# Performance work log

Measured on AMD Instinct MI355X. Metric: run time of the kernel, lower is better.

## Reference

```python
import jax, jax.numpy as jnp
import numpy as np

N_HEAD = 16
N_KV = 4
HEAD_DIM = 128
EPS = 1e-6


def setup_inputs() -> dict:
    key = jax.random.key(0)
    k1, k2, k3 = jax.random.split(key, 3)
    d_model = N_HEAD * HEAD_DIM
    qkv_out = (N_HEAD + 2 * N_KV) * HEAD_DIM
    B, T = 2, 2048
    x = jax.random.normal(k1, (B, T, d_model), dtype=jnp.float32)
    W_qkv = jax.random.normal(k2, (d_model, qkv_out), dtype=jnp.float32) * (d_model ** -0.5)
    W_proj = jax.random.normal(k3, (d_model, d_model), dtype=jnp.float32) * (d_model ** -0.5)
    q_scale = jnp.ones((HEAD_DIM,), dtype=jnp.float32)
    k_scale = jnp.ones((HEAD_DIM,), dtype=jnp.float32)
    return {"x": x, "W_qkv": W_qkv, "W_proj": W_proj, "q_scale": q_scale, "k_scale": k_scale}


def _rms_norm(t):
    return t * jax.lax.rsqrt(jnp.mean(t * t, axis=-1, keepdims=True) + EPS)


def reference(x, W_qkv, W_proj, q_scale, k_scale):
    B, T, C = x.shape
    qkv = x @ W_qkv  # [B, T, (H+2*KV)*D]
    q, k, v = jnp.split(qkv, [N_HEAD * HEAD_DIM, (N_HEAD + N_KV) * HEAD_DIM], axis=-1)
    q = q.reshape(B, T, N_HEAD, HEAD_DIM).transpose(0, 2, 1, 3)  # [B,H,T,D]
    k = k.reshape(B, T, N_KV, HEAD_DIM).transpose(0, 2, 1, 3)    # [B,KV,T,D]
    v = v.reshape(B, T, N_KV, HEAD_DIM).transpose(0, 2, 1, 3)
    # QK RMS-norm with learned per-dim scales
    q = _rms_norm(q) * q_scale
    k = _rms_norm(k) * k_scale
    # GQA: repeat kv heads to match query heads
    rep = N_HEAD // N_KV
    k = jnp.repeat(k, rep, axis=1)
    v = jnp.repeat(v, rep, axis=1)
    # causal SDPA
    scale = 1.0 / jnp.sqrt(jnp.float32(HEAD_DIM))
    scores = jnp.einsum('bhqd,bhkd->bhqk', q, k) * scale
    causal = jnp.tril(jnp.ones((T, T), dtype=bool))
    scores = jnp.where(causal, scores, jnp.finfo(scores.dtype).min)
    attn = jax.nn.softmax(scores, axis=-1)
    y = jnp.einsum('bhqk,bhkd->bhqd', attn, v)  # [B,H,T,D]
    y = y.transpose(0, 2, 1, 3).reshape(B, T, C)
    return y @ W_proj
```

## Files before the change

kernel.cpp:

```cpp
#include <hip/hip_runtime.h>

typedef __bf16 bf16;
typedef __bf16 bf16x8 __attribute__((ext_vector_type(8)));
typedef __bf16 bf16x4 __attribute__((ext_vector_type(4)));
typedef float f32x4 __attribute__((ext_vector_type(4)));
typedef float f32x16 __attribute__((ext_vector_type(16)));
typedef unsigned u32x4 __attribute__((ext_vector_type(4)));

#define EXP2F(x) __builtin_amdgcn_exp2f(x)

#define LOAD_LDS16(gp, lp)                                                     \
  __builtin_amdgcn_global_load_lds(                                            \
      (const __attribute__((address_space(1))) void*)(gp),                     \
      (__attribute__((address_space(3))) void*)(lp), 16, 0, 0)

__global__ __launch_bounds__(256) void k_pre(const float* __restrict__ x,
                                             const float* __restrict__ Wqkv,
                                             bf16* __restrict__ xb,
                                             bf16* __restrict__ Wqkvt) {
  int bid = blockIdx.x, tid = threadIdx.x;
  if (bid < 4096) {
    int i = bid * 256 + tid;
    float4 v0 = ((const float4*)x)[2 * i];
    float4 v1 = ((const float4*)x)[2 * i + 1];
    bf16x8 o = {(bf16)v0.x, (bf16)v0.y, (bf16)v0.z, (bf16)v0.w,
                (bf16)v1.x, (bf16)v1.y, (bf16)v1.z, (bf16)v1.w};
    ((bf16x8*)xb)[i] = o;
    return;
  }
  __shared__ bf16 t[64 * 65];
  int f = bid - 4096;
  int c0 = (f % 48) * 64, r0 = (f / 48) * 64;
  const int C = 3072, R = 2048;
#pragma unroll
  for (int i = 0; i < 16; ++i) {
    int f2 = i * 256 + tid;
    int rl = f2 >> 6, cl = f2 & 63;
    t[rl * 65 + cl] = (bf16)Wqkv[(size_t)(r0 + rl) * C + c0 + cl];
  }
  __syncthreads();
#pragma unroll
  for (int i = 0; i < 4; ++i) {
    int idx = i * 256 + tid;
    int cl = idx >> 4, rl0 = (idx & 15) * 4;
    bf16x4 o = {t[(rl0 + 0) * 65 + cl], t[(rl0 + 1) * 65 + cl],
                t[(rl0 + 2) * 65 + cl], t[(rl0 + 3) * 65 + cl]};
    *(bf16x4*)&Wqkvt[(size_t)(c0 + cl) * R + r0 + rl0] = o;
  }
}

template <typename OutT, int BM>
__global__ __launch_bounds__(512, 2) void k_gemm256(const bf16* __restrict__ A,
                                                    const bf16* __restrict__ Bt,
                                                    OutT* __restrict__ C,
                                                    int M, int N, int K,
                                                    const float* __restrict__ Wp,
                                                    bf16* __restrict__ Wpt) {
  constexpr int ASZ = 4 * BM * 8;
  constexpr int MREP = BM / 32;
  __shared__ alignas(16) bf16 As[2][2][ASZ];
  __shared__ alignas(16) bf16 Bs[2][2][4 * 256 * 8];
  int tid = threadIdx.x;
  int wid = tid >> 6, lane = tid & 63;
  int g = lane >> 4, lr = lane & 15;
  int wrow = (wid >> 2) * (BM / 2), wcol = (wid & 3) * 64;
  int gx = gridDim.x;
  int flat = blockIdx.y * gx + blockIdx.x;
  int ntiles = (M / BM) * (N / 256);
  if (flat >= ntiles) {
    bf16* t = (bf16*)&As[0][0][0];
    int b2 = flat - ntiles;
    for (int k = 0; k < 16; ++k) {
      int st = b2 * 16 + k;
      int c0 = (st & 31) * 64, r0 = (st >> 5) * 64;
#pragma unroll
      for (int i = 0; i < 8; ++i) {
        int f2 = i * 512 + tid;
        int rl = f2 >> 6, cl = f2 & 63;
        t[rl * 65 + cl] = (bf16)Wp[(size_t)(r0 + rl) * 2048 + c0 + cl];
      }
      __syncthreads();
#pragma unroll
      for (int i = 0; i < 2; ++i) {
        int idx = i * 512 + tid;
        int cl = idx >> 4, rl0 = (idx & 15) * 4;
        bf16x4 o = {t[(rl0 + 0) * 65 + cl], t[(rl0 + 1) * 65 + cl],
                    t[(rl0 + 2) * 65 + cl], t[(rl0 + 3) * 65 + cl]};
        *(bf16x4*)&Wpt[(size_t)(c0 + cl) * 2048 + r0 + rl0] = o;
      }
      __syncthreads();
    }
    return;
  }
  int cpx = ntiles >> 3;
  int f2 = (flat & 7) * cpx + (flat >> 3);
  int row0 = (f2 % gx) * BM, col0 = (f2 / gx) * 256;
  int NT = K >> 6;
  f32x4 acc[MREP][4] = {};

  auto stageA = [&](int buf, int kh, int kt) {
#pragma unroll
    for (int pass = 0; pass < BM / 128; ++pass) {
      int slot = pass * 512 + tid;
      int kseg, row;
      if constexpr (BM == 256) { kseg = slot >> 8; row = slot & 255; }
      else { kseg = slot >> 7; row = slot & 127; }
      LOAD_LDS16(A + (size_t)(row0 + row) * K + kt * 64 + kh * 32 + kseg * 8,
                 &As[buf][kh][slot * 8]);
    }
  };
  auto stageB = [&](int buf, int kh, int kt) {
#pragma unroll
    for (int pass = 0; pass < 2; ++pass) {
      int slot = pass * 512 + tid;
      int kseg = slot >> 8, row = slot & 255;
      LOAD_LDS16(Bt + (size_t)(col0 + row) * K + kt * 64 + kh * 32 + kseg * 8,
                 &Bs[buf][kh][slot * 8]);
    }
  };
  auto dsA = [&](int buf, int s, int mq, bf16x8* af) {
#pragma unroll
    for (int i = 0; i < 4; ++i)
      af[i] = *(const bf16x8*)&As[buf][s]
                  [(g * BM + wrow + (mq * 4 + i) * 16 + lr) * 8];
  };
  auto dsB = [&](int buf, int s, bf16x8* bfr) {
#pragma unroll
    for (int i = 0; i < 4; ++i)
      bfr[i] = *(const bf16x8*)&Bs[buf][s][((g << 8) + wcol + i * 16 + lr) * 8];
  };
  auto mfma16 = [&](int mq, bf16x8* af, bf16x8* bfr) {
    __builtin_amdgcn_s_setprio(1);
#pragma unroll
    for (int i = 0; i < 4; ++i)
#pragma unroll
      for (int n = 0; n < 4; ++n)
        acc[mq * 4 + i][n] = __builtin_amdgcn_mfma_f32_16x16x32_bf16(
            af[i], bfr[n], acc[mq * 4 + i][n], 0, 0, 0);
    __builtin_amdgcn_s_setprio(0);
  };

  stageA(0, 0, 0);
  stageB(0, 0, 0);
  stageA(0, 1, 0);
  stageB(0, 1, 0);
  if constexpr (BM == 256)
    asm volatile("s_waitcnt vmcnt(4)" ::: "memory");
  else
    asm volatile("s_waitcnt vmcnt(3)" ::: "memory");
  __builtin_amdgcn_s_barrier();

  for (int T = 0; T < NT; ++T) {
    int buf = T & 1, nbuf = buf ^ 1;
    bool more = (T + 1 < NT);
    bf16x8 af[4], bfr[4];
    if constexpr (BM == 256) {
      dsA(buf, 0, 0, af);
      dsB(buf, 0, bfr);
      if (more) stageA(nbuf, 0, T + 1);
      __builtin_amdgcn_s_barrier();
      mfma16(0, af, bfr);
      __builtin_amdgcn_s_barrier();
      dsA(buf, 0, 1, af);
      if (more) {
        stageB(nbuf, 0, T + 1);
        asm volatile("s_waitcnt vmcnt(4)" ::: "memory");
      } else {
        asm volatile("s_waitcnt vmcnt(0)" ::: "memory");
      }
      __builtin_amdgcn_s_barrier();
      mfma16(1, af, bfr);
      __builtin_amdgcn_s_barrier();
      dsA(buf, 1, 0, af);
      dsB(buf, 1, bfr);
      if (more) stageA(nbuf, 1, T + 1);
      __builtin_amdgcn_s_barrier();
      mfma16(0, af, bfr);
      __builtin_amdgcn_s_barrier();
      dsA(buf, 1, 1, af);
      if (more) {
        stageB(nbuf, 1, T + 1);
        asm volatile("s_waitcnt vmcnt(4)" ::: "memory");
      }
      __builtin_amdgcn_s_barrier();
      mfma16(1, af, bfr);
      __builtin_amdgcn_s_barrier();
    } else {
      dsA(buf, 0, 0, af);
      dsB(buf, 0, bfr);
      if (more) {
        stageA(nbuf, 0, T + 1);
        stageB(nbuf, 0, T + 1);
        asm volatile("s_waitcnt vmcnt(3)" ::: "memory");
      } else {
        asm volatile("s_waitcnt vmcnt(0)" ::: "memory");
      }
      __builtin_amdgcn_s_barrier();
      mfma16(0, af, bfr);
      __builtin_amdgcn_s_barrier();
      dsA(buf, 1, 0, af);
      dsB(buf, 1, bfr);
      if (more) {
        stageA(nbuf, 1, T + 1);
        stageB(nbuf, 1, T + 1);
        asm volatile("s_waitcnt vmcnt(3)" ::: "memory");
      }
      __builtin_amdgcn_s_barrier();
      mfma16(0, af, bfr);
      __builtin_amdgcn_s_barrier();
    }
  }

#pragma unroll
  for (int mi = 0; mi < MREP; ++mi)
#pragma unroll
    for (int ni = 0; ni < 4; ++ni) {
      int rb = row0 + wrow + mi * 16 + g * 4;
      int cc = col0 + wcol + ni * 16 + lr;
#pragma unroll
      for (int r = 0; r < 4; ++r) C[(size_t)(rb + r) * N + cc] = (OutT)acc[mi][ni][r];
    }
}

__global__ __launch_bounds__(256) void k_post(bf16* __restrict__ qkv,
                                              const float* __restrict__ ks,
                                              bf16* __restrict__ Vt) {
  int bid = blockIdx.x, tid = threadIdx.x;
  if (bid < 1024) {
    int wid = tid >> 6, lane = tid & 63;
    int tok = bid * 4 + wid;
    int d = lane * 2;
    bf16* rowp = qkv + (size_t)tok * 3072 + 2048;
#pragma unroll
    for (int kvh = 0; kvh < 4; ++kvh) {
      int cb = kvh * 128;
      float v0 = (float)rowp[cb + d], v1 = (float)rowp[cb + d + 1];
      float ss = v0 * v0 + v1 * v1;
#pragma unroll
      for (int off = 1; off < 64; off <<= 1) ss += __shfl_xor(ss, off);
      float r = rsqrtf(ss * (1.0f / 128.0f) + 1e-6f);
      rowp[cb + d] = (bf16)(v0 * r * ks[d]);
      rowp[cb + d + 1] = (bf16)(v1 * r * ks[d + 1]);
    }
    return;
  }
  __shared__ bf16 t[64 * 65];
  int f = bid - 1024;
  int t0 = (f & 31) * 64;
  int d0 = ((f >> 5) & 1) * 64;
  int bh = f >> 6;
  int b = bh >> 2, kvh = bh & 3;
  const bf16* src = qkv + (size_t)(b * 2048) * 3072 + 2560 + kvh * 128;
  bf16* dst = Vt + (size_t)bh * 262144 + (size_t)(t0 >> 6) * 8192;
#pragma unroll
  for (int i = 0; i < 16; ++i) {
    int ff = i * 256 + tid;
    int tl = ff >> 6, dl = ff & 63;
    t[tl * 65 + dl] = src[(size_t)(t0 + tl) * 3072 + d0 + dl];
  }
  __syncthreads();
#pragma unroll
  for (int i = 0; i < 2; ++i) {
    int v = i * 256 + tid;
    int c = v >> 6, dv = v & 63;
    bf16x8 o;
#pragma unroll
    for (int j = 0; j < 8; ++j) o[j] = t[(c * 8 + j) * 65 + dv];
    *(bf16x8*)&dst[(size_t)c * 1024 + (size_t)(d0 + dv) * 8] = o;
  }
}

__device__ inline unsigned pack2bf(float a, float b) {
  union { bf16 h[2]; unsigned u; } x;
  x.h[0] = (bf16)a;
  x.h[1] = (bf16)b;
  return x.u;
}

__global__ __launch_bounds__(256, 2) void k_attn(const bf16* __restrict__ qkv,
                                                 const bf16* __restrict__ Vt,
                                                 bf16* __restrict__ y,
                                                 const float* __restrict__ qs) {
  int flat = blockIdx.x;
  int slot = flat >> 8;
  int j = flat & 255;
  int xcd = j & 7, iw = j >> 3;
  int h = xcd + 8 * (iw & 1);
  int r = iw >> 1;
  int b = r & 1;
  int qt = slot ? (r >> 1) : (15 - (r >> 1));
  int kvh = h >> 2;
  int tid = threadIdx.x;
  int wid = tid >> 6, lane = tid & 63;
  int qc = lane & 31, hi = lane >> 5;
  __shared__ alignas(16) bf16 Ks[2][16 * 64 * 8];
  __shared__ alignas(16) bf16 Vs[2][8 * 128 * 8];
  __shared__ float sqs[128];
  const bf16* Qb = qkv + (size_t)(b * 2048) * 3072 + h * 128;
  const bf16* Kb = qkv + (size_t)(b * 2048) * 3072 + 2048 + kvh * 128;
  const bf16* Vb = Vt + (size_t)(b * 4 + kvh) * 262144;
  int qw0 = qt * 128 + wid * 32;
  int qg = qw0 + qc;
  if (tid < 128)
    sqs[tid] = qs[tid] * (0.08838834764831845f * 1.4426950408889634f);
  __syncthreads();
  bf16x8 qf[8];
#pragma unroll
  for (int s = 0; s < 8; ++s)
    qf[s] = *(const bf16x8*)&Qb[(size_t)qg * 3072 + s * 16 + hi * 8];
  float ssq = 0.f;
#pragma unroll
  for (int s = 0; s < 8; ++s)
#pragma unroll
    for (int jj = 0; jj < 8; ++jj) {
      float v = (float)qf[s][jj];
      ssq += v * v;
    }
  ssq += __shfl_xor(ssq, 32);
  float qrms = rsqrtf(ssq * (1.0f / 128.0f) + 1e-6f);
#pragma unroll
  for (int s = 0; s < 8; ++s)
#pragma unroll
    for (int jj = 0; jj < 8; ++jj)
      qf[s][jj] = (bf16)((float)qf[s][jj] * qrms * sqs[s * 16 + hi * 8 + jj]);
  f32x16 acc[4] = {};
  float mrun = -1e30f, lrun = 0.f;

  auto STAGE = [&](int buf, int kt2) {
    int s0 = kt2 * 64;
#pragma unroll
    for (int i = 0; i < 4; ++i) {
      int sl = i * 256 + tid;
      int ch = sl >> 6, row = sl & 63;
      LOAD_LDS16(Kb + (size_t)(s0 + row) * 3072 + ch * 8, &Ks[buf][sl * 8]);
    }
#pragma unroll
    for (int i = 0; i < 4; ++i) {
      int sl = i * 256 + tid;
      LOAD_LDS16(Vb + (size_t)kt2 * 8192 + sl * 8, &Vs[buf][sl * 8]);
    }
  };

  STAGE(0, 0);
  int cur = 0;
  int ktmax = 2 * qt + 1;
  for (int kt = 0; kt <= ktmax; ++kt) {
    int s0 = kt * 64;
    if (kt < ktmax) {
      STAGE(cur ^ 1, kt + 1);
      asm volatile("s_waitcnt vmcnt(8)" ::: "memory");
    } else {
      asm volatile("s_waitcnt vmcnt(0)" ::: "memory");
    }
    __builtin_amdgcn_s_barrier();
    __builtin_amdgcn_sched_barrier(0);
    if (s0 <= qw0 + 31) {
      f32x16 sc[2] = {};
      __builtin_amdgcn_s_setprio(1);
#pragma unroll
      for (int s = 0; s < 8; ++s)
#pragma unroll
        for (int n = 0; n < 2; ++n) {
          bf16x8 kf =
              *(const bf16x8*)&Ks[cur][(((2 * s + hi) << 6) + n * 32 + qc) * 8];
          sc[n] =
              __builtin_amdgcn_mfma_f32_32x32x16_bf16(kf, qf[s], sc[n], 0, 0, 0);
        }
      __builtin_amdgcn_s_setprio(0);
      if (s0 + 63 > qw0) {
#pragma unroll
        for (int n = 0; n < 2; ++n)
#pragma unroll
          for (int r2 = 0; r2 < 16; ++r2) {
            int kg = s0 + n * 32 + (r2 & 3) + 8 * (r2 >> 2) + 4 * hi;
            if (kg > qg) sc[n][r2] = -1e30f;
          }
      }
      float pm = -1e30f;
#pragma unroll
      for (int n = 0; n < 2; ++n)
#pragma unroll
        for (int r2 = 0; r2 < 16; ++r2) pm = fmaxf(pm, sc[n][r2]);
      pm = fmaxf(pm, __shfl_xor(pm, 32));
      if (__any(pm > mrun + 11.0f)) {
        float mnew = fmaxf(mrun, pm);
        float scl = EXP2F(mrun - mnew);
        mrun = mnew;
        lrun *= scl;
        float sv[16];
#pragma unroll
        for (int r2 = 0; r2 < 16; ++r2)
          sv[r2] = __shfl(scl, (r2 & 3) + 8 * (r2 >> 2) + 4 * hi);
#pragma unroll
        for (int dt = 0; dt < 4; ++dt)
#pragma unroll
          for (int r2 = 0; r2 < 16; ++r2) acc[dt][r2] *= sv[r2];
      }
      float rs = 0.f;
#pragma unroll
      for (int n = 0; n < 2; ++n) {
        unsigned pk[8];
#pragma unroll
        for (int mm = 0; mm < 8; ++mm) {
          float e0 = EXP2F(sc[n][2 * mm] - mrun);
          float e1 = EXP2F(sc[n][2 * mm + 1] - mrun);
          rs += e0 + e1;
          pk[mm] = pack2bf(e0, e1);
        }
#pragma unroll
        for (int l2 = 0; l2 < 2; ++l2) {
          unsigned a0 = pk[4 * l2 + 0], b0 = pk[4 * l2 + 2];
          unsigned a1 = pk[4 * l2 + 1], b1 = pk[4 * l2 + 3];
          asm volatile("v_permlane32_swap_b32 %0, %1" : "+v"(a0), "+v"(b0));
          asm volatile("v_permlane32_swap_b32 %0, %1" : "+v"(a1), "+v"(b1));
          u32x4 w = {a0, a1, b0, b1};
          bf16x8 pf = __builtin_bit_cast(bf16x8, w);
          int c = 2 * (2 * n + l2) + hi;
          __builtin_amdgcn_s_setprio(1);
#pragma unroll
          for (int dt = 0; dt < 4; ++dt) {
            bf16x8 vf =
                *(const bf16x8*)&Vs[cur][((c << 7) + dt * 32 + qc) * 8];
            acc[dt] =
                __builtin_amdgcn_mfma_f32_32x32x16_bf16(pf, vf, acc[dt], 0, 0, 0);
          }
          __builtin_amdgcn_s_setprio(0);
        }
      }
      rs += __shfl_xor(rs, 32);
      lrun += rs;
    }
    __builtin_amdgcn_sched_barrier(0);
    __builtin_amdgcn_s_barrier();
    cur ^= 1;
  }
  float rlv = 1.0f / lrun;
  float rcl[16];
#pragma unroll
  for (int r2 = 0; r2 < 16; ++r2)
    rcl[r2] = __shfl(rlv, (r2 & 3) + 8 * (r2 >> 2) + 4 * hi);
#pragma unroll
  for (int dt = 0; dt < 4; ++dt)
#pragma unroll
    for (int r2 = 0; r2 < 16; ++r2) {
      int row = qw0 + (r2 & 3) + 8 * (r2 >> 2) + 4 * hi;
      float v = acc[dt][r2] * rcl[r2];
      y[(size_t)(b * 2048 + row) * 2048 + h * 128 + dt * 32 + qc] = (bf16)v;
    }
}

extern "C" void kernel_launch(void* const* d_in, const int* in_sizes, int n_in,
                              void* d_out, int out_size, void* d_ws,
                              size_t ws_size, hipStream_t stream) {
  const float* x = (const float*)d_in[0];
  const float* Wqkv = (const float*)d_in[1];
  const float* Wproj = (const float*)d_in[2];
  const float* qs = (const float*)d_in[3];
  const float* ks = (const float*)d_in[4];
  float* out = (float*)d_out;
  char* ws = (char*)d_ws;

  bf16* xb = (bf16*)(ws);
  bf16* Wqkvt = (bf16*)(ws + (size_t)(16u << 20));
  bf16* Wprojt = (bf16*)(ws + (size_t)(28u << 20));
  bf16* qkv = (bf16*)(ws + (size_t)(36u << 20));
  bf16* Vt = Wqkvt;
  bf16* y = xb;

  k_pre<<<5632, 256, 0, stream>>>(x, Wqkv, xb, Wqkvt);
  k_gemm256<bf16, 256><<<dim3(16, 16), 512, 0, stream>>>(
      xb, Wqkvt, qkv, 4096, 3072, 2048, Wproj, Wprojt);
  k_post<<<1536, 256, 0, stream>>>(qkv, ks, Vt);
  k_attn<<<dim3(512, 1, 1), 256, 0, stream>>>(qkv, Vt, y, qs);
  k_gemm256<float, 128><<<dim3(32, 8), 512, 0, stream>>>(
      y, Wprojt, out, 4096, 2048, 2048, nullptr, nullptr);
}
```

Baseline: 237.7 us.

## Fuse V transpose into QKV GEMM epilogue and drop separate transpose pass

The QKV GEMM epilogue now writes the V columns directly in the blocked, transposed layout the attention kernel expects, stored in place within the qkv buffer. The k_post kernel no longer does the LDS-based V transpose and only applies the K RMS-norm. The attention kernel's V staging loads read from that region of qkv. This removes one read and one write pass over V and shrinks a launch, at the cost of strided bf16x4 stores in the GEMM epilogue and larger-stride V loads in attention.

```diff
diff --git a/kernel.cpp b/kernel.cpp
--- a/kernel.cpp
+++ b/kernel.cpp
@@ -211,6 +211,23 @@
     }
   }
 
+  if (col0 >= 2560) {
+#pragma unroll
+    for (int mi = 0; mi < MREP; ++mi)
+#pragma unroll
+      for (int ni = 0; ni < 4; ++ni) {
+        int vcol = col0 + wcol + ni * 16 + lr - 2560;
+        int kvh = vcol >> 7, d = vcol & 127;
+        int t0r = row0 + wrow + mi * 16 + g * 4;
+        int rowp = (t0r & ~7) + (d >> 4);
+        int colp = 2560 + kvh * 128 + (d & 15) * 8 + (t0r & 7);
+        bf16x4 o = {(bf16)acc[mi][ni][0], (bf16)acc[mi][ni][1],
+                    (bf16)acc[mi][ni][2], (bf16)acc[mi][ni][3]};
+        *(bf16x4*)&((bf16*)C)[(size_t)rowp * N + colp] = o;
+      }
+    return;
+  }
+
 #pragma unroll
   for (int mi = 0; mi < MREP; ++mi)
 #pragma unroll
@@ -223,50 +240,22 @@
 }
 
 __global__ __launch_bounds__(256) void k_post(bf16* __restrict__ qkv,
-                                              const float* __restrict__ ks,
-                                              bf16* __restrict__ Vt) {
+                                              const float* __restrict__ ks) {
   int bid = blockIdx.x, tid = threadIdx.x;
-  if (bid < 1024) {
-    int wid = tid >> 6, lane = tid & 63;
-    int tok = bid * 4 + wid;
-    int d = lane * 2;
-    bf16* rowp = qkv + (size_t)tok * 3072 + 2048;
-#pragma unroll
-    for (int kvh = 0; kvh < 4; ++kvh) {
-      int cb = kvh * 128;
-      float v0 = (float)rowp[cb + d], v1 = (float)rowp[cb + d + 1];
-      float ss = v0 * v0 + v1 * v1;
-#pragma unroll
-      for (int off = 1; off < 64; off <<= 1) ss += __shfl_xor(ss, off);
-      float r = rsqrtf(ss * (1.0f / 128.0f) + 1e-6f);
-      rowp[cb + d] = (bf16)(v0 * r * ks[d]);
-      rowp[cb + d + 1] = (bf16)(v1 * r * ks[d + 1]);
-    }
-    return;
-  }
-  __shared__ bf16 t[64 * 65];
-  int f = bid - 1024;
-  int t0 = (f & 31) * 64;
-  int d0 = ((f >> 5) & 1) * 64;
-  int bh = f >> 6;
-  int b = bh >> 2, kvh = bh & 3;
-  const bf16* src = qkv + (size_t)(b * 2048) * 3072 + 2560 + kvh * 128;
-  bf16* dst = Vt + (size_t)bh * 262144 + (size_t)(t0 >> 6) * 8192;
-#pragma unroll
-  for (int i = 0; i < 16; ++i) {
-    int ff = i * 256 + tid;
-    int tl = ff >> 6, dl = ff & 63;
-    t[tl * 65 + dl] = src[(size_t)(t0 + tl) * 3072 + d0 + dl];
-  }
-  __syncthreads();
-#pragma unroll
-  for (int i = 0; i < 2; ++i) {
-    int v = i * 256 + tid;
-    int c = v >> 6, dv = v & 63;
-    bf16x8 o;
-#pragma unroll
-    for (int j = 0; j < 8; ++j) o[j] = t[(c * 8 + j) * 65 + dv];
-    *(bf16x8*)&dst[(size_t)c * 1024 + (size_t)(d0 + dv) * 8] = o;
+  int wid = tid >> 6, lane = tid & 63;
+  int tok = bid * 4 + wid;
+  int d = lane * 2;
+  bf16* rowp = qkv + (size_t)tok * 3072 + 2048;
+#pragma unroll
+  for (int kvh = 0; kvh < 4; ++kvh) {
+    int cb = kvh * 128;
+    float v0 = (float)rowp[cb + d], v1 = (float)rowp[cb + d + 1];
+    float ss = v0 * v0 + v1 * v1;
+#pragma unroll
+    for (int off = 1; off < 64; off <<= 1) ss += __shfl_xor(ss, off);
+    float r = rsqrtf(ss * (1.0f / 128.0f) + 1e-6f);
+    rowp[cb + d] = (bf16)(v0 * r * ks[d]);
+    rowp[cb + d + 1] = (bf16)(v1 * r * ks[d + 1]);
   }
 }
 
@@ -278,7 +267,6 @@
 }
 
 __global__ __launch_bounds__(256, 2) void k_attn(const bf16* __restrict__ qkv,
-                                                 const bf16* __restrict__ Vt,
                                                  bf16* __restrict__ y,
                                                  const float* __restrict__ qs) {
   int flat = blockIdx.x;
@@ -298,7 +286,7 @@
   __shared__ float sqs[128];
   const bf16* Qb = qkv + (size_t)(b * 2048) * 3072 + h * 128;
   const bf16* Kb = qkv + (size_t)(b * 2048) * 3072 + 2048 + kvh * 128;
-  const bf16* Vb = Vt + (size_t)(b * 4 + kvh) * 262144;
+  const bf16* Vb = qkv + (size_t)(b * 2048) * 3072 + 2560 + kvh * 128;
   int qw0 = qt * 128 + wid * 32;
   int qg = qw0 + qc;
   if (tid < 128)
@@ -337,7 +325,8 @@
 #pragma unroll
     for (int i = 0; i < 4; ++i) {
       int sl = i * 256 + tid;
-      LOAD_LDS16(Vb + (size_t)kt2 * 8192 + sl * 8, &Vs[buf][sl * 8]);
+      LOAD_LDS16(Vb + (size_t)(s0 + (sl >> 4)) * 3072 + (sl & 15) * 8,
+                 &Vs[buf][sl * 8]);
     }
   };
 
@@ -464,14 +453,13 @@
   bf16* Wqkvt = (bf16*)(ws + (size_t)(16u << 20));
   bf16* Wprojt = (bf16*)(ws + (size_t)(28u << 20));
   bf16* qkv = (bf16*)(ws + (size_t)(36u << 20));
-  bf16* Vt = Wqkvt;
   bf16* y = xb;
 
   k_pre<<<5632, 256, 0, stream>>>(x, Wqkv, xb, Wqkvt);
   k_gemm256<bf16, 256><<<dim3(16, 16), 512, 0, stream>>>(
       xb, Wqkvt, qkv, 4096, 3072, 2048, Wproj, Wprojt);
-  k_post<<<1536, 256, 0, stream>>>(qkv, ks, Vt);
-  k_attn<<<dim3(512, 1, 1), 256, 0, stream>>>(qkv, Vt, y, qs);
+  k_post<<<1024, 256, 0, stream>>>(qkv, ks);
+  k_attn<<<dim3(512, 1, 1), 256, 0, stream>>>(qkv, y, qs);
   k_gemm256<float, 128><<<dim3(32, 8), 512, 0, stream>>>(
       y, Wprojt, out, 4096, 2048, 2048, nullptr, nullptr);
 }
```

Measured after the change: 239.2 us. No clear change (+0.6%).
